# Kernel tuning notes

Hardware: AMD Instinct MI355X
Metric: run time of the kernel (lower is better)

The kernel has to match this reference:

```python
import jax, jax.numpy as jnp
import numpy as np

SIZE = 256
D_IN = 256
EPS = 1e-3  # keras BatchNormalization default epsilon


def _mlp(x, W1, b1, W2, b2):
    # smallMLP: Dense(size, relu) -> Dense(size)
    return jax.nn.relu(x @ W1 + b1) @ W2 + b2


def setup_inputs() -> dict:
    key = jax.random.key(0)
    ks = jax.random.split(key, 20)
    B, L1, L2 = 16, 1024, 1024
    s = 0.02
    inp = {
        "seq1M": jax.random.normal(ks[0], (B, L1, D_IN), jnp.float32),
        "seq2M": jax.random.normal(ks[1], (B, L2, D_IN), jnp.float32),
        "distogram": jax.random.uniform(ks[2], (B, L1, L2), jnp.float32),
        # shared K/Q/V smallMLP params (same layers applied to seq1 and seq2)
        "kW1": jax.random.normal(ks[3], (D_IN, SIZE), jnp.float32) * s,
        "kb1": jnp.zeros((SIZE,), jnp.float32),
        "kW2": jax.random.normal(ks[4], (SIZE, SIZE), jnp.float32) * s,
        "kb2": jnp.zeros((SIZE,), jnp.float32),
        "qW1": jax.random.normal(ks[5], (D_IN, SIZE), jnp.float32) * s,
        "qb1": jnp.zeros((SIZE,), jnp.float32),
        "qW2": jax.random.normal(ks[6], (SIZE, SIZE), jnp.float32) * s,
        "qb2": jnp.zeros((SIZE,), jnp.float32),
        "vW1": jax.random.normal(ks[7], (D_IN, SIZE), jnp.float32) * s,
        "vb1": jnp.zeros((SIZE,), jnp.float32),
        "vW2": jax.random.normal(ks[8], (SIZE, SIZE), jnp.float32) * s,
        "vb2": jnp.zeros((SIZE,), jnp.float32),
        # output projections
        "fc1W": jax.random.normal(ks[9], (SIZE, SIZE), jnp.float32) * s,
        "fc1b": jnp.zeros((SIZE,), jnp.float32),
        "fc2W": jax.random.normal(ks[10], (SIZE, SIZE), jnp.float32) * s,
        "fc2b": jnp.zeros((SIZE,), jnp.float32),
        # shared BatchNorm (inference mode, moving stats)
        "bn_gamma": jnp.ones((SIZE,), jnp.float32),
        "bn_beta": jnp.zeros((SIZE,), jnp.float32),
        "bn_mean": jnp.zeros((SIZE,), jnp.float32),
        "bn_var": jnp.ones((SIZE,), jnp.float32),
    }
    return inp


def reference(seq1M, seq2M, distogram,
              kW1, kb1, kW2, kb2,
              qW1, qb1, qW2, qb2,
              vW1, vb1, vW2, vb2,
              fc1W, fc1b, fc2W, fc2b,
              bn_gamma, bn_beta, bn_mean, bn_var):
    size = jnp.float32(SIZE)
    k1 = _mlp(seq1M, kW1, kb1, kW2, kb2)   # [B, L1, S]
    q1 = _mlp(seq1M, qW1, qb1, qW2, qb2)
    v1 = _mlp(seq1M, vW1, vb1, vW2, vb2)
    k2 = _mlp(seq2M, kW1, kb1, kW2, kb2)   # [B, L2, S]
    q2 = _mlp(seq2M, qW1, qb1, qW2, qb2)
    v2 = _mlp(seq2M, vW1, vb1, vW2, vb2)

    # distogram-scaled scores, softmax over axis 1 (query axis — non-standard)
    scores1 = jnp.einsum('bls,bms->blm', q1, k2) * distogram / size  # [B, L1, L2]
    w1 = jax.nn.softmax(scores1, axis=1)
    scores2 = jnp.einsum('bms,bls->bml', q2, k1) * jnp.transpose(distogram, (0, 2, 1)) / size  # [B, L2, L1]
    w2 = jax.nn.softmax(scores2, axis=1)

    # transpose(matmul(V^T, W), [0,2,1]) == einsum contracting the softmax axis
    ap1 = jnp.einsum('bls,blm->bms', v1, w1)  # [B, L2, S]
    ap2 = jnp.einsum('bms,bml->bls', v2, w2)  # [B, L1, S]

    def bn(x):
        return (x - bn_mean) * jax.lax.rsqrt(bn_var + EPS) * bn_gamma + bn_beta

    out1 = bn(jax.nn.relu(ap1 @ fc1W + fc1b))
    out2 = bn(jax.nn.relu(ap2 @ fc2W + fc2b))
    return out1, out2
```

## Files before the change

kernel.cpp:

```cpp
#include <hip/hip_runtime.h>
#include <hip/hip_bf16.h>


typedef __attribute__((ext_vector_type(8))) short bf16x8;
typedef __attribute__((ext_vector_type(4))) float f32x4;
typedef unsigned short u16;

__device__ __forceinline__ unsigned int f2bfbits(float f) {
  union { float f; unsigned int i; } v; v.f = f;
  return (v.i + 0x7fffu + ((v.i >> 16) & 1u)) >> 16;
}
__device__ __forceinline__ unsigned int pk2(float a, float b) {
  return f2bfbits(a) | (f2bfbits(b) << 16);
}

__global__ void pack_wt(const float* __restrict__ w0, const float* __restrict__ w1,
                        const float* __restrict__ w2, const float* __restrict__ w3,
                        const float* __restrict__ w4, const float* __restrict__ w5,
                        const float* __restrict__ w6, const float* __restrict__ w7,
                        u16* __restrict__ out) {
  const float* wsel[8] = {w0, w1, w2, w3, w4, w5, w6, w7};
  const float* W = wsel[blockIdx.y];
  u16* o = out + (size_t)blockIdx.y * 65536;
  int i0 = blockIdx.x * 1024 + threadIdx.x * 4;
  int n = i0 >> 8, k = i0 & 255;
  float a = W[(k + 0) * 256 + n];
  float b = W[(k + 1) * 256 + n];
  float c = W[(k + 2) * 256 + n];
  float d = W[(k + 3) * 256 + n];
  uint2 pv;
  pv.x = pk2(a, b);
  pv.y = pk2(c, d);
  *(uint2*)(o + i0) = pv;
}

__global__ __launch_bounds__(256, 2)
void mlp3_fused(const float* __restrict__ seqA, const float* __restrict__ seqB,
                const u16* __restrict__ Wt8,
                const float* __restrict__ kb1, const float* __restrict__ kb2,
                const float* __restrict__ qb1, const float* __restrict__ qb2,
                const float* __restrict__ vb1, const float* __restrict__ vb2,
                u16* __restrict__ kA, u16* __restrict__ qA, u16* __restrict__ vA,
                u16* __restrict__ kB, u16* __restrict__ qB, u16* __restrict__ vB)
{
  __shared__ u16 As[64][256];
  __shared__ u16 Hl[64][256];

  const int tid = threadIdx.x;
  const int lane = tid & 63;
  const int w = tid >> 6;
  const int l15 = lane & 15, lq = lane >> 4;
  const int seqsel = blockIdx.x >> 8;
  const size_t m0 = (size_t)(blockIdx.x & 255) * 64;
  const float* __restrict__ seq = seqsel ? seqB : seqA;

  {
    const int row = tid >> 2, cg = tid & 3;
    const float* src = seq + (m0 + row) * 256 + cg * 64;
#pragma unroll
    for (int cc = 0; cc < 8; ++cc) {
      float4 f0 = *(const float4*)(src + cc * 8);
      float4 f1 = *(const float4*)(src + cc * 8 + 4);
      uint4 pk;
      pk.x = pk2(f0.x, f0.y);
      pk.y = pk2(f0.z, f0.w);
      pk.z = pk2(f1.x, f1.y);
      pk.w = pk2(f1.z, f1.w);
      const int ch = (cg * 8 + cc) ^ (row & 7);
      *(uint4*)&As[row][ch * 8] = pk;
    }
  }
  __syncthreads();

#pragma unroll
  for (int mlp = 0; mlp < 3; ++mlp) {
    const u16* __restrict__ W1 = Wt8 + (size_t)(mlp * 2) * 65536;
    const u16* __restrict__ W2 = Wt8 + (size_t)(mlp * 2 + 1) * 65536;
    const float* __restrict__ b1 = (mlp == 0) ? kb1 : (mlp == 1) ? qb1 : vb1;
    const float* __restrict__ b2 = (mlp == 0) ? kb2 : (mlp == 1) ? qb2 : vb2;
    u16* __restrict__ dst =
        (mlp == 0) ? (seqsel ? kB : kA) : (mlp == 1) ? (seqsel ? qB : qA) : (seqsel ? vB : vA);

    float b1v[4][4];
#pragma unroll
    for (int ni = 0; ni < 4; ++ni)
#pragma unroll
      for (int r = 0; r < 4; ++r) b1v[ni][r] = b1[w * 64 + ni * 16 + 4 * lq + r];
    float b2v[4];
#pragma unroll
    for (int ni = 0; ni < 4; ++ni) b2v[ni] = b2[w * 64 + ni * 16 + l15];

    f32x4 a1[4][4];
#pragma unroll
    for (int ni = 0; ni < 4; ++ni)
#pragma unroll
      for (int mj = 0; mj < 4; ++mj) a1[ni][mj] = (f32x4)0.0f;
#pragma unroll
    for (int ks = 0; ks < 8; ++ks) {
      bf16x8 wf[4], af[4];
#pragma unroll
      for (int ni = 0; ni < 4; ++ni)
        wf[ni] = *(const bf16x8*)(W1 + (size_t)(w * 64 + ni * 16 + l15) * 256 + ks * 32 + lq * 8);
#pragma unroll
      for (int mj = 0; mj < 4; ++mj) {
        const int row = mj * 16 + l15;
        const int ch = (ks * 4 + lq) ^ (row & 7);
        af[mj] = *(const bf16x8*)&As[row][ch * 8];
      }
#pragma unroll
      for (int ni = 0; ni < 4; ++ni)
#pragma unroll
        for (int mj = 0; mj < 4; ++mj)
          a1[ni][mj] = __builtin_amdgcn_mfma_f32_16x16x32_bf16(wf[ni], af[mj], a1[ni][mj], 0, 0, 0);
    }

    __syncthreads();
#pragma unroll
    for (int ni = 0; ni < 4; ++ni) {
      const int chl = w * 8 + ni * 2 + (lq >> 1);
#pragma unroll
      for (int mj = 0; mj < 4; ++mj) {
        const int m = mj * 16 + l15;
        float h0 = fmaxf(a1[ni][mj][0] + b1v[ni][0], 0.f);
        float h1 = fmaxf(a1[ni][mj][1] + b1v[ni][1], 0.f);
        float h2 = fmaxf(a1[ni][mj][2] + b1v[ni][2], 0.f);
        float h3 = fmaxf(a1[ni][mj][3] + b1v[ni][3], 0.f);
        uint2 pv;
        pv.x = pk2(h0, h1);
        pv.y = pk2(h2, h3);
        const int ch = chl ^ (m & 7);
        *(uint2*)&Hl[m][ch * 8 + (lq & 1) * 4] = pv;
      }
    }
    __syncthreads();

    f32x4 a2[4][4];
#pragma unroll
    for (int mi = 0; mi < 4; ++mi)
#pragma unroll
      for (int ni = 0; ni < 4; ++ni) a2[mi][ni] = (f32x4)0.0f;
#pragma unroll
    for (int ks = 0; ks < 8; ++ks) {
      bf16x8 wf[4], hf[4];
#pragma unroll
      for (int ni = 0; ni < 4; ++ni)
        wf[ni] = *(const bf16x8*)(W2 + (size_t)(w * 64 + ni * 16 + l15) * 256 + ks * 32 + lq * 8);
#pragma unroll
      for (int mi = 0; mi < 4; ++mi) {
        const int row = mi * 16 + l15;
        const int ch = (ks * 4 + lq) ^ (row & 7);
        hf[mi] = *(const bf16x8*)&Hl[row][ch * 8];
      }
#pragma unroll
      for (int mi = 0; mi < 4; ++mi)
#pragma unroll
        for (int ni = 0; ni < 4; ++ni)
          a2[mi][ni] = __builtin_amdgcn_mfma_f32_16x16x32_bf16(hf[mi], wf[ni], a2[mi][ni], 0, 0, 0);
    }

#pragma unroll
    for (int ni = 0; ni < 4; ++ni) {
      const int col = w * 64 + ni * 16 + l15;
      const float bb = b2v[ni];
#pragma unroll
      for (int mi = 0; mi < 4; ++mi) {
        const size_t grow0 = m0 + mi * 16 + 4 * lq;
        float z[4];
#pragma unroll
        for (int r = 0; r < 4; ++r) z[r] = a2[mi][ni][r] + bb;
        if (mlp != 2) {
#pragma unroll
          for (int r = 0; r < 4; ++r)
            dst[(grow0 + r) * 256 + col] = (u16)f2bfbits(z[r]);
        } else {
          uint2 pv;
          pv.x = pk2(z[0], z[1]);
          pv.y = pk2(z[2], z[3]);
          const size_t bb2 = grow0 >> 10, lrow = grow0 & 1023;
          *(uint2*)(dst + ((size_t)bb2 * 256 + col) * 1024 + lrow) = pv;
        }
      }
    }
  }
}

enum { EPI_RELU_BF16 = 0, EPI_BF16 = 1, EPI_VT = 2, EPI_BN = 3 };

template <bool AF32, int EPI>
__global__ __launch_bounds__(256, 2)
void gemm_mfma(const void* __restrict__ Aptr, const u16* __restrict__ Wt,
               const float* __restrict__ bias, void* __restrict__ Cout,
               const float* __restrict__ bn_g, const float* __restrict__ bn_b,
               const float* __restrict__ bn_m, const float* __restrict__ bn_v)
{
  __shared__ u16 As[128][64];
  __shared__ u16 Ws[64][64];
  const int tid = threadIdx.x;
  const int lane = tid & 63;
  const int w = tid >> 6;
  const int wr = w >> 1, wc = w & 1;
  const int l15 = lane & 15, lq = lane >> 4;
  const size_t bm = (size_t)blockIdx.x * 128;
  const int bn = blockIdx.y * 64;

  const int sar = tid >> 1, sah = tid & 1;
  const int swr = tid >> 2, swc = tid & 3;

  f32x4 acc[4][2];
#pragma unroll
  for (int mi = 0; mi < 4; ++mi)
#pragma unroll
    for (int ni = 0; ni < 2; ++ni) acc[mi][ni] = (f32x4)0.0f;

  for (int k0 = 0; k0 < 256; k0 += 64) {
    __syncthreads();
    if (AF32) {
      const float* A = (const float*)Aptr + (bm + sar) * 256 + k0 + sah * 32;
#pragma unroll
      for (int c = 0; c < 4; ++c) {
        float4 f0 = *(const float4*)(A + c * 8);
        float4 f1 = *(const float4*)(A + c * 8 + 4);
        uint4 pk;
        pk.x = pk2(f0.x, f0.y);
        pk.y = pk2(f0.z, f0.w);
        pk.z = pk2(f1.x, f1.y);
        pk.w = pk2(f1.z, f1.w);
        int cc = (sah * 4 + c) ^ (sar & 7);
        *(uint4*)&As[sar][cc * 8] = pk;
      }
    } else {
      const u16* A = (const u16*)Aptr + (bm + sar) * 256 + k0 + sah * 32;
#pragma unroll
      for (int c = 0; c < 4; ++c) {
        uint4 v = *(const uint4*)(A + c * 8);
        int cc = (sah * 4 + c) ^ (sar & 7);
        *(uint4*)&As[sar][cc * 8] = v;
      }
    }
    {
      const u16* Wp = Wt + (size_t)(bn + swr) * 256 + k0 + swc * 16;
#pragma unroll
      for (int c = 0; c < 2; ++c) {
        uint4 v = *(const uint4*)(Wp + c * 8);
        int cc = (swc * 2 + c) ^ (swr & 7);
        *(uint4*)&Ws[swr][cc * 8] = v;
      }
    }
    __syncthreads();
#pragma unroll
    for (int ks = 0; ks < 2; ++ks) {
      bf16x8 af[4], wf[2];
#pragma unroll
      for (int mi = 0; mi < 4; ++mi) {
        int row = wr * 64 + mi * 16 + l15;
        int cc = (ks * 4 + lq) ^ (row & 7);
        af[mi] = *(const bf16x8*)&As[row][cc * 8];
      }
#pragma unroll
      for (int ni = 0; ni < 2; ++ni) {
        int row = wc * 32 + ni * 16 + l15;
        int cc = (ks * 4 + lq) ^ (row & 7);
        wf[ni] = *(const bf16x8*)&Ws[row][cc * 8];
      }
#pragma unroll
      for (int mi = 0; mi < 4; ++mi)
#pragma unroll
        for (int ni = 0; ni < 2; ++ni)
          acc[mi][ni] = __builtin_amdgcn_mfma_f32_16x16x32_bf16(
              af[mi], wf[ni], acc[mi][ni], 0, 0, 0);
    }
  }

#pragma unroll
  for (int ni = 0; ni < 2; ++ni) {
    const int col = bn + wc * 32 + ni * 16 + l15;
    const float bi = bias[col];
    float g = 0.f, be = 0.f, mu = 0.f, iv = 0.f;
    if (EPI == EPI_BN) {
      g = bn_g[col];
      be = bn_b[col];
      mu = bn_m[col];
      iv = rsqrtf(bn_v[col] + 1e-3f);
    }
#pragma unroll
    for (int mi = 0; mi < 4; ++mi) {
      const size_t grow0 = bm + wr * 64 + mi * 16 + 4 * lq;
      float z[4];
#pragma unroll
      for (int r = 0; r < 4; ++r) z[r] = acc[mi][ni][r] + bi;
      if (EPI == EPI_RELU_BF16) {
#pragma unroll
        for (int r = 0; r < 4; ++r)
          ((u16*)Cout)[(grow0 + r) * 256 + col] = (u16)f2bfbits(fmaxf(z[r], 0.f));
      } else if (EPI == EPI_BF16) {
#pragma unroll
        for (int r = 0; r < 4; ++r)
          ((u16*)Cout)[(grow0 + r) * 256 + col] = (u16)f2bfbits(z[r]);
      } else if (EPI == EPI_VT) {
        uint2 pv;
        pv.x = pk2(z[0], z[1]);
        pv.y = pk2(z[2], z[3]);
        const size_t b = grow0 >> 10, lrow = grow0 & 1023;
        *(uint2*)((u16*)Cout + ((size_t)b * 256 + col) * 1024 + lrow) = pv;
      } else {
#pragma unroll
        for (int r = 0; r < 4; ++r) {
          float zz = fmaxf(z[r], 0.f);
          ((float*)Cout)[(grow0 + r) * 256 + col] = (zz - mu) * iv * g + be;
        }
      }
    }
  }
}

__global__ __launch_bounds__(256, 2)
void attn_mfma(const u16* __restrict__ Qa, const u16* __restrict__ Ka,
               const u16* __restrict__ Va, u16* __restrict__ OutA,
               const u16* __restrict__ Qb, const u16* __restrict__ Kb,
               const u16* __restrict__ Vb, u16* __restrict__ OutB,
               const float* __restrict__ D2)
{
  __shared__ union U {
    struct {
      u16 Ks[2][32][256];
      u16 Vts[2][256][32];
      u16 Pl[64][40];
    } s;
    u16 Osw[4][16][264];
  } u;

  const int orig = blockIdx.x;
  const int lid = (orig & 7) * 64 + (orig >> 3);
  const int dir = lid >> 8;
  const int b = (lid >> 4) & 15;
  const int i0 = (lid & 15) * 64;

  const u16* __restrict__ Q = dir ? Qb : Qa;
  const u16* __restrict__ K = dir ? Kb : Ka;
  const u16* __restrict__ Vt = dir ? Vb : Va;
  u16* __restrict__ Out = dir ? OutB : OutA;

  const int tid = threadIdx.x;
  const int lane = tid & 63;
  const int w = tid >> 6;
  const int l15 = lane & 15, lq = lane >> 4;
  const size_t sbase = (size_t)b * (1024 * 256);
  const size_t vtbase = (size_t)b * (256 * 1024);
  const size_t dbase = (size_t)b * (1024 * 1024);

  bf16x8 q[8];
  {
    const u16* Qp = Q + sbase + (size_t)(i0 + w * 16 + l15) * 256 + lq * 8;
#pragma unroll
    for (int ks = 0; ks < 8; ++ks) q[ks] = *(const bf16x8*)(Qp + ks * 32);
  }

  const int cb0 = w * 4;
  auto stage = [&](int bi, int j0) {
#pragma unroll
    for (int i = 0; i < 4; ++i) {
      const int cb = cb0 + i;
      {
        const int krow = cb * 2 + (lane >> 5);
        const int kch = (lane & 31) ^ (krow & 7);
        const u16* gs = K + sbase + (size_t)(j0 + krow) * 256 + kch * 8;
        __builtin_amdgcn_global_load_lds(
            (const __attribute__((address_space(1))) unsigned int*)gs,
            (__attribute__((address_space(3))) unsigned int*)&u.s.Ks[bi][cb * 2][0],
            16, 0, 0);
      }
      {
        const int vrow = cb * 16 + (lane >> 2);
        const int vch = lane & 3;
        const u16* gs = Vt + vtbase + (size_t)vrow * 1024 + j0 + ((vch ^ (vrow & 3)) * 8);
        __builtin_amdgcn_global_load_lds(
            (const __attribute__((address_space(1))) unsigned int*)gs,
            (__attribute__((address_space(3))) unsigned int*)&u.s.Vts[bi][cb * 16][0],
            16, 0, 0);
      }
    }
  };

  float mrow[4], lsum[4];
  f32x4 o[16];
#pragma unroll
  for (int r = 0; r < 4; ++r) { mrow[r] = -1e30f; lsum[r] = 0.f; }
#pragma unroll
  for (int nt = 0; nt < 16; ++nt) o[nt] = (f32x4)0.0f;

  stage(0, 0);

  const int vcc = lq ^ (l15 & 3);

  for (int t = 0; t < 32; ++t) {
    const int bi = t & 1;
    const int j0 = t * 32;

    float breg[8];
    if (dir == 0) {
#pragma unroll
      for (int nt = 0; nt < 2; ++nt)
#pragma unroll
        for (int r = 0; r < 4; ++r)
          breg[nt * 4 + r] =
              D2[dbase + (size_t)(j0 + l15 + 16 * nt) * 1024 + (i0 + w * 16 + 4 * lq + r)];
    } else {
#pragma unroll
      for (int nt = 0; nt < 2; ++nt)
#pragma unroll
        for (int r = 0; r < 4; ++r)
          breg[nt * 4 + r] =
              D2[dbase + (size_t)(i0 + w * 16 + 4 * lq + r) * 1024 + j0 + l15 + 16 * nt];
    }

    if (t + 1 < 32) {
      stage(bi ^ 1, j0 + 32);
      asm volatile("s_waitcnt vmcnt(16)" ::: "memory");
    } else {
      asm volatile("s_waitcnt vmcnt(0)" ::: "memory");
    }
    __builtin_amdgcn_s_barrier();
    __builtin_amdgcn_sched_barrier(0);

    f32x4 sa[2];
    sa[0] = (f32x4)0.0f;
    sa[1] = (f32x4)0.0f;
#pragma unroll
    for (int ks = 0; ks < 8; ++ks)
#pragma unroll
      for (int nt = 0; nt < 2; ++nt) {
        const int row = nt * 16 + l15;
        const int cc = (ks * 4 + lq) ^ (row & 7);
        bf16x8 kb = *(const bf16x8*)&u.s.Ks[bi][row][cc * 8];
        sa[nt] = __builtin_amdgcn_mfma_f32_16x16x32_bf16(q[ks], kb, sa[nt], 0, 0, 0);
      }

    float s0[4], s1[4];
    bool need = false;
#pragma unroll
    for (int r = 0; r < 4; ++r) {
      s0[r] = sa[0][r] * breg[r] * 0.00390625f;
      s1[r] = sa[1][r] * breg[4 + r] * 0.00390625f;
      need = need || (s0[r] > mrow[r] + 8.f) || (s1[r] > mrow[r] + 8.f);
    }
    if (__any(need)) {
#pragma unroll
      for (int r = 0; r < 4; ++r) {
        float mx = fmaxf(s0[r], s1[r]);
        mx = fmaxf(mx, __shfl_xor(mx, 1, 16));
        mx = fmaxf(mx, __shfl_xor(mx, 2, 16));
        mx = fmaxf(mx, __shfl_xor(mx, 4, 16));
        mx = fmaxf(mx, __shfl_xor(mx, 8, 16));
        const float mn = fmaxf(mrow[r], mx);
        const float sc = __expf(mrow[r] - mn);
        mrow[r] = mn;
        lsum[r] *= sc;
#pragma unroll
        for (int nt = 0; nt < 16; ++nt) o[nt][r] *= sc;
      }
    }
    float p0v[4], p1v[4];
#pragma unroll
    for (int r = 0; r < 4; ++r) {
      p0v[r] = __expf(s0[r] - mrow[r]);
      p1v[r] = __expf(s1[r] - mrow[r]);
      lsum[r] += p0v[r] + p1v[r];
    }
#pragma unroll
    for (int r = 0; r < 4; ++r) {
      const int qrow = w * 16 + 4 * lq + r;
      u.s.Pl[qrow][l15] = (u16)f2bfbits(p0v[r]);
      u.s.Pl[qrow][16 + l15] = (u16)f2bfbits(p1v[r]);
    }
    __threadfence_block();
    const bf16x8 pa = *(const bf16x8*)&u.s.Pl[w * 16 + l15][lq * 8];

#pragma unroll
    for (int nt = 0; nt < 16; ++nt) {
      bf16x8 vb = *(const bf16x8*)&u.s.Vts[bi][nt * 16 + l15][vcc * 8];
      o[nt] = __builtin_amdgcn_mfma_f32_16x16x32_bf16(pa, vb, o[nt], 0, 0, 0);
    }

    asm volatile("s_waitcnt lgkmcnt(0)" ::: "memory");
    __builtin_amdgcn_s_barrier();
  }

  float inv[4];
#pragma unroll
  for (int r = 0; r < 4; ++r) {
    float rs = lsum[r];
    rs += __shfl_xor(rs, 1, 16);
    rs += __shfl_xor(rs, 2, 16);
    rs += __shfl_xor(rs, 4, 16);
    rs += __shfl_xor(rs, 8, 16);
    inv[r] = 1.0f / rs;
  }
#pragma unroll
  for (int nt = 0; nt < 16; ++nt) {
#pragma unroll
    for (int r = 0; r < 4; ++r)
      u.Osw[w][4 * lq + r][nt * 16 + l15] = (u16)f2bfbits(o[nt][r] * inv[r]);
  }
  __threadfence_block();
  {
    const int orow = lane >> 2, och = (lane & 3) * 64;
    const u16* src = &u.Osw[w][orow][och];
    u16* dst = Out + sbase + (size_t)(i0 + w * 16 + orow) * 256 + och;
#pragma unroll
    for (int c = 0; c < 8; ++c) *(uint4*)(dst + c * 8) = *(const uint4*)(src + c * 8);
  }
}

extern "C" void kernel_launch(void* const* d_in, const int* in_sizes, int n_in,
                              void* d_out, int out_size, void* d_ws, size_t ws_size,
                              hipStream_t stream)
{
  (void)in_sizes; (void)n_in; (void)out_size; (void)ws_size;

  const float* seq1  = (const float*)d_in[0];
  const float* seq2  = (const float*)d_in[1];
  const float* disto = (const float*)d_in[2];
  const float* kW1 = (const float*)d_in[3];
  const float* kb1 = (const float*)d_in[4];
  const float* kW2 = (const float*)d_in[5];
  const float* kb2 = (const float*)d_in[6];
  const float* qW1 = (const float*)d_in[7];
  const float* qb1 = (const float*)d_in[8];
  const float* qW2 = (const float*)d_in[9];
  const float* qb2 = (const float*)d_in[10];
  const float* vW1 = (const float*)d_in[11];
  const float* vb1 = (const float*)d_in[12];
  const float* vW2 = (const float*)d_in[13];
  const float* vb2 = (const float*)d_in[14];
  const float* fc1W = (const float*)d_in[15];
  const float* fc1b = (const float*)d_in[16];
  const float* fc2W = (const float*)d_in[17];
  const float* fc2b = (const float*)d_in[18];
  const float* bn_g = (const float*)d_in[19];
  const float* bn_b = (const float*)d_in[20];
  const float* bn_m = (const float*)d_in[21];
  const float* bn_v = (const float*)d_in[22];

  char* ws = (char*)d_ws;
  const size_t MB = 1024 * 1024;
  u16* Wt8 = (u16*)(ws);
  u16* k1  = (u16*)(ws + 1 * MB);
  u16* q1  = (u16*)(ws + 9 * MB);
  u16* k2  = (u16*)(ws + 17 * MB);
  u16* q2  = (u16*)(ws + 25 * MB);
  u16* v1t = (u16*)(ws + 33 * MB);
  u16* v2t = (u16*)(ws + 41 * MB);
  u16* ap1 = (u16*)(ws + 49 * MB);
  u16* ap2 = (u16*)(ws + 57 * MB);

  pack_wt<<<dim3(64, 8), 256, 0, stream>>>(kW1, kW2, qW1, qW2, vW1, vW2, fc1W, fc2W, Wt8);

  mlp3_fused<<<dim3(512), dim3(256), 0, stream>>>(
      seq1, seq2, Wt8, kb1, kb2, qb1, qb2, vb1, vb2,
      k1, q1, v1t, k2, q2, v2t);

  attn_mfma<<<dim3(512), dim3(256), 0, stream>>>(
      k2, q1, v1t, ap1,
      k1, q2, v2t, ap2,
      disto);

  float* out1 = (float*)d_out;
  float* out2 = (float*)d_out + 4194304;
  dim3 ggrid(128, 4), gblk(256);
  gemm_mfma<false, EPI_BN><<<ggrid, gblk, 0, stream>>>(
      ap1, Wt8 + 6ull * 65536, fc1b, (void*)out1, bn_g, bn_b, bn_m, bn_v);
  gemm_mfma<false, EPI_BN><<<ggrid, gblk, 0, stream>>>(
      ap2, Wt8 + 7ull * 65536, fc2b, (void*)out2, bn_g, bn_b, bn_m, bn_v);
}
```

Measured before the change: 184.0 us.

## Vectorize transposed distogram loads via LDS transpose, add MFMA priority hints

For direction 0, where the distogram tile is read transposed, each lane now issues two float4 loads along the contiguous dimension instead of eight scattered scalar loads, then transposes the values through a small per-wave LDS buffer. The vmcnt wait is adjusted to match the smaller number of outstanding loads. s_setprio raises wave priority around both MFMA loops, and __threadfence_block is replaced by an explicit lgkmcnt wait plus sched_barrier. The extra LDS use may lower occupancy, and the LDS round-trip adds latency.

```diff
diff --git a/kernel.cpp b/kernel.cpp
--- a/kernel.cpp
+++ b/kernel.cpp
@@ -325,6 +325,7 @@
       u16 Ks[2][32][256];
       u16 Vts[2][256][32];
       u16 Pl[64][40];
+      float Pw[4][32][20];
     } s;
     u16 Osw[4][16][264];
   } u;
@@ -391,19 +392,18 @@
   stage(0, 0);
 
   const int vcc = lq ^ (l15 & 3);
+  const int bj = lane & 31, bh = lane >> 5;
 
   for (int t = 0; t < 32; ++t) {
     const int bi = t & 1;
     const int j0 = t * 32;
 
     float breg[8];
+    float4 bb0, bb1;
     if (dir == 0) {
-#pragma unroll
-      for (int nt = 0; nt < 2; ++nt)
-#pragma unroll
-        for (int r = 0; r < 4; ++r)
-          breg[nt * 4 + r] =
-              D2[dbase + (size_t)(j0 + l15 + 16 * nt) * 1024 + (i0 + w * 16 + 4 * lq + r)];
+      const float* bsrc = D2 + dbase + (size_t)(j0 + bj) * 1024 + i0 + w * 16 + bh * 8;
+      bb0 = *(const float4*)bsrc;
+      bb1 = *(const float4*)(bsrc + 4);
     } else {
 #pragma unroll
       for (int nt = 0; nt < 2; ++nt)
@@ -415,16 +415,26 @@
 
     if (t + 1 < 32) {
       stage(bi ^ 1, j0 + 32);
-      asm volatile("s_waitcnt vmcnt(16)" ::: "memory");
+      if (dir == 0)
+        asm volatile("s_waitcnt vmcnt(10)" ::: "memory");
+      else
+        asm volatile("s_waitcnt vmcnt(16)" ::: "memory");
     } else {
       asm volatile("s_waitcnt vmcnt(0)" ::: "memory");
     }
     __builtin_amdgcn_s_barrier();
     __builtin_amdgcn_sched_barrier(0);
+
+    if (dir == 0) {
+      float* pw = &u.s.Pw[w][bj][bh * 8];
+      *(float4*)pw = bb0;
+      *(float4*)(pw + 4) = bb1;
+    }
 
     f32x4 sa[2];
     sa[0] = (f32x4)0.0f;
     sa[1] = (f32x4)0.0f;
+    __builtin_amdgcn_s_setprio(1);
 #pragma unroll
     for (int ks = 0; ks < 8; ++ks)
 #pragma unroll
@@ -434,13 +444,22 @@
         bf16x8 kb = *(const bf16x8*)&u.s.Ks[bi][row][cc * 8];
         sa[nt] = __builtin_amdgcn_mfma_f32_16x16x32_bf16(q[ks], kb, sa[nt], 0, 0, 0);
       }
+    __builtin_amdgcn_s_setprio(0);
 
     float s0[4], s1[4];
     bool need = false;
 #pragma unroll
     for (int r = 0; r < 4; ++r) {
-      s0[r] = sa[0][r] * breg[r] * 0.00390625f;
-      s1[r] = sa[1][r] * breg[4 + r] * 0.00390625f;
+      float b0, b1;
+      if (dir == 0) {
+        b0 = u.s.Pw[w][l15][4 * lq + r];
+        b1 = u.s.Pw[w][l15 + 16][4 * lq + r];
+      } else {
+        b0 = breg[r];
+        b1 = breg[4 + r];
+      }
+      s0[r] = sa[0][r] * b0 * 0.00390625f;
+      s1[r] = sa[1][r] * b1 * 0.00390625f;
       need = need || (s0[r] > mrow[r] + 8.f) || (s1[r] > mrow[r] + 8.f);
     }
     if (__any(need)) {
@@ -472,14 +491,17 @@
       u.s.Pl[qrow][l15] = (u16)f2bfbits(p0v[r]);
       u.s.Pl[qrow][16 + l15] = (u16)f2bfbits(p1v[r]);
     }
-    __threadfence_block();
+    asm volatile("s_waitcnt lgkmcnt(0)" ::: "memory");
+    __builtin_amdgcn_sched_barrier(0);
     const bf16x8 pa = *(const bf16x8*)&u.s.Pl[w * 16 + l15][lq * 8];
 
+    __builtin_amdgcn_s_setprio(1);
 #pragma unroll
     for (int nt = 0; nt < 16; ++nt) {
       bf16x8 vb = *(const bf16x8*)&u.s.Vts[bi][nt * 16 + l15][vcc * 8];
       o[nt] = __builtin_amdgcn_mfma_f32_16x16x32_bf16(pa, vb, o[nt], 0, 0, 0);
     }
+    __builtin_amdgcn_s_setprio(0);
 
     asm volatile("s_waitcnt lgkmcnt(0)" ::: "memory");
     __builtin_amdgcn_s_barrier();
@@ -501,7 +523,8 @@
     for (int r = 0; r < 4; ++r)
       u.Osw[w][4 * lq + r][nt * 16 + l15] = (u16)f2bfbits(o[nt][r] * inv[r]);
   }
-  __threadfence_block();
+  asm volatile("s_waitcnt lgkmcnt(0)" ::: "memory");
+  __builtin_amdgcn_sched_barrier(0);
   {
     const int orow = lane >> 2, och = (lane & 3) * 64;
     const u16* src = &u.Osw[w][orow][och];
```

Measured after the change: 261.1 us. 41.9% more time.

## Pre-transpose distogram to bf16 and restructure K/V staging in attention

Applied to the files above, without the earlier changes.

Adds a pack_disto kernel that transposes the distogram to bf16, so direction-0 attention reads it row-contiguously instead of with strided column reads. V staging becomes single-buffered and is issued at the start of each iteration, with a mid-iteration barrier and vmcnt waits replacing the fence, so V loads overlap the QK MFMAs. It also raises wave priority around the MFMA blocks with s_setprio. This trades an extra full pass over the 64MB distogram plus bf16 rounding of the scale against cheaper loads and less LDS inside the attention loop.

```diff
diff --git a/kernel.cpp b/kernel.cpp
--- a/kernel.cpp
+++ b/kernel.cpp
@@ -12,6 +12,11 @@
 }
 __device__ __forceinline__ unsigned int pk2(float a, float b) {
   return f2bfbits(a) | (f2bfbits(b) << 16);
+}
+__device__ __forceinline__ float bf2f(u16 x) {
+  union { unsigned int i; float f; } v;
+  v.i = (unsigned int)x << 16;
+  return v.f;
 }
 
 __global__ void pack_wt(const float* __restrict__ w0, const float* __restrict__ w1,
@@ -34,6 +39,32 @@
   *(uint2*)(o + i0) = pv;
 }
 
+__global__ __launch_bounds__(256)
+void pack_disto(const float* __restrict__ D, u16* __restrict__ Dt) {
+  __shared__ u16 T[64][72];
+  const int b = blockIdx.z, l0 = blockIdx.y * 64, m0 = blockIdx.x * 64;
+  const float* src = D + (size_t)b * (1024 * 1024);
+  u16* dst = Dt + (size_t)b * (1024 * 1024);
+  const int r = threadIdx.x >> 2, c0 = (threadIdx.x & 3) * 16;
+  float4 f[4];
+#pragma unroll
+  for (int q = 0; q < 4; ++q)
+    f[q] = *(const float4*)(src + (size_t)(l0 + r) * 1024 + m0 + c0 + q * 4);
+  uint4 p0, p1;
+  p0.x = pk2(f[0].x, f[0].y); p0.y = pk2(f[0].z, f[0].w);
+  p0.z = pk2(f[1].x, f[1].y); p0.w = pk2(f[1].z, f[1].w);
+  p1.x = pk2(f[2].x, f[2].y); p1.y = pk2(f[2].z, f[2].w);
+  p1.z = pk2(f[3].x, f[3].y); p1.w = pk2(f[3].z, f[3].w);
+  *(uint4*)&T[r][c0] = p0;
+  *(uint4*)&T[r][c0 + 8] = p1;
+  __syncthreads();
+  u16 vals[16];
+#pragma unroll
+  for (int k = 0; k < 16; ++k) vals[k] = T[c0 + k][r];
+  *(uint4*)(dst + (size_t)(m0 + r) * 1024 + l0 + c0) = *(uint4*)&vals[0];
+  *(uint4*)(dst + (size_t)(m0 + r) * 1024 + l0 + c0 + 8) = *(uint4*)&vals[8];
+}
+
 __global__ __launch_bounds__(256, 2)
 void mlp3_fused(const float* __restrict__ seqA, const float* __restrict__ seqB,
                 const u16* __restrict__ Wt8,
@@ -318,12 +349,12 @@
                const u16* __restrict__ Va, u16* __restrict__ OutA,
                const u16* __restrict__ Qb, const u16* __restrict__ Kb,
                const u16* __restrict__ Vb, u16* __restrict__ OutB,
-               const float* __restrict__ D2)
+               const u16* __restrict__ D1t, const float* __restrict__ D2)
 {
   __shared__ union U {
     struct {
       u16 Ks[2][32][256];
-      u16 Vts[2][256][32];
+      u16 Vts[256][32];
       u16 Pl[64][40];
     } s;
     u16 Osw[4][16][264];
@@ -356,28 +387,30 @@
   }
 
   const int cb0 = w * 4;
-  auto stage = [&](int bi, int j0) {
+  auto stage_K = [&](int bi, int j0) {
 #pragma unroll
     for (int i = 0; i < 4; ++i) {
       const int cb = cb0 + i;
-      {
-        const int krow = cb * 2 + (lane >> 5);
-        const int kch = (lane & 31) ^ (krow & 7);
-        const u16* gs = K + sbase + (size_t)(j0 + krow) * 256 + kch * 8;
-        __builtin_amdgcn_global_load_lds(
-            (const __attribute__((address_space(1))) unsigned int*)gs,
-            (__attribute__((address_space(3))) unsigned int*)&u.s.Ks[bi][cb * 2][0],
-            16, 0, 0);
-      }
-      {
-        const int vrow = cb * 16 + (lane >> 2);
-        const int vch = lane & 3;
-        const u16* gs = Vt + vtbase + (size_t)vrow * 1024 + j0 + ((vch ^ (vrow & 3)) * 8);
-        __builtin_amdgcn_global_load_lds(
-            (const __attribute__((address_space(1))) unsigned int*)gs,
-            (__attribute__((address_space(3))) unsigned int*)&u.s.Vts[bi][cb * 16][0],
-            16, 0, 0);
-      }
+      const int krow = cb * 2 + (lane >> 5);
+      const int kch = (lane & 31) ^ (krow & 7);
+      const u16* gs = K + sbase + (size_t)(j0 + krow) * 256 + kch * 8;
+      __builtin_amdgcn_global_load_lds(
+          (const __attribute__((address_space(1))) unsigned int*)gs,
+          (__attribute__((address_space(3))) unsigned int*)&u.s.Ks[bi][cb * 2][0],
+          16, 0, 0);
+    }
+  };
+  auto stage_V = [&](int j0) {
+#pragma unroll
+    for (int i = 0; i < 4; ++i) {
+      const int cb = cb0 + i;
+      const int vrow = cb * 16 + (lane >> 2);
+      const int vch = lane & 3;
+      const u16* gs = Vt + vtbase + (size_t)vrow * 1024 + j0 + ((vch ^ (vrow & 3)) * 8);
+      __builtin_amdgcn_global_load_lds(
+          (const __attribute__((address_space(1))) unsigned int*)gs,
+          (__attribute__((address_space(3))) unsigned int*)&u.s.Vts[cb * 16][0],
+          16, 0, 0);
     }
   };
 
@@ -388,7 +421,7 @@
 #pragma unroll
   for (int nt = 0; nt < 16; ++nt) o[nt] = (f32x4)0.0f;
 
-  stage(0, 0);
+  stage_K(0, 0);
 
   const int vcc = lq ^ (l15 & 3);
 
@@ -396,28 +429,31 @@
     const int bi = t & 1;
     const int j0 = t * 32;
 
-    float breg[8];
+    u16 bregu[8];
+    float bregf[8];
     if (dir == 0) {
 #pragma unroll
       for (int nt = 0; nt < 2; ++nt)
 #pragma unroll
         for (int r = 0; r < 4; ++r)
-          breg[nt * 4 + r] =
-              D2[dbase + (size_t)(j0 + l15 + 16 * nt) * 1024 + (i0 + w * 16 + 4 * lq + r)];
+          bregu[nt * 4 + r] =
+              D1t[dbase + (size_t)(i0 + w * 16 + 4 * lq + r) * 1024 + j0 + l15 + 16 * nt];
     } else {
 #pragma unroll
       for (int nt = 0; nt < 2; ++nt)
 #pragma unroll
         for (int r = 0; r < 4; ++r)
-          breg[nt * 4 + r] =
+          bregf[nt * 4 + r] =
               D2[dbase + (size_t)(i0 + w * 16 + 4 * lq + r) * 1024 + j0 + l15 + 16 * nt];
     }
 
+    stage_V(j0);
+    __builtin_amdgcn_sched_barrier(0);
     if (t + 1 < 32) {
-      stage(bi ^ 1, j0 + 32);
+      stage_K(bi ^ 1, j0 + 32);
       asm volatile("s_waitcnt vmcnt(16)" ::: "memory");
     } else {
-      asm volatile("s_waitcnt vmcnt(0)" ::: "memory");
+      asm volatile("s_waitcnt vmcnt(12)" ::: "memory");
     }
     __builtin_amdgcn_s_barrier();
     __builtin_amdgcn_sched_barrier(0);
@@ -425,6 +461,7 @@
     f32x4 sa[2];
     sa[0] = (f32x4)0.0f;
     sa[1] = (f32x4)0.0f;
+    __builtin_amdgcn_s_setprio(1);
 #pragma unroll
     for (int ks = 0; ks < 8; ++ks)
 #pragma unroll
@@ -434,13 +471,16 @@
         bf16x8 kb = *(const bf16x8*)&u.s.Ks[bi][row][cc * 8];
         sa[nt] = __builtin_amdgcn_mfma_f32_16x16x32_bf16(q[ks], kb, sa[nt], 0, 0, 0);
       }
+    __builtin_amdgcn_s_setprio(0);
 
     float s0[4], s1[4];
     bool need = false;
 #pragma unroll
     for (int r = 0; r < 4; ++r) {
-      s0[r] = sa[0][r] * breg[r] * 0.00390625f;
-      s1[r] = sa[1][r] * breg[4 + r] * 0.00390625f;
+      const float b0 = (dir == 0) ? bf2f(bregu[r]) : bregf[r];
+      const float b1 = (dir == 0) ? bf2f(bregu[4 + r]) : bregf[4 + r];
+      s0[r] = sa[0][r] * b0 * 0.00390625f;
+      s1[r] = sa[1][r] * b1 * 0.00390625f;
       need = need || (s0[r] > mrow[r] + 8.f) || (s1[r] > mrow[r] + 8.f);
     }
     if (__any(need)) {
@@ -472,14 +512,21 @@
       u.s.Pl[qrow][l15] = (u16)f2bfbits(p0v[r]);
       u.s.Pl[qrow][16 + l15] = (u16)f2bfbits(p1v[r]);
     }
-    __threadfence_block();
+    if (t + 1 < 32)
+      asm volatile("s_waitcnt vmcnt(4) lgkmcnt(0)" ::: "memory");
+    else
+      asm volatile("s_waitcnt vmcnt(0) lgkmcnt(0)" ::: "memory");
+    __builtin_amdgcn_sched_barrier(0);
+    __builtin_amdgcn_s_barrier();
     const bf16x8 pa = *(const bf16x8*)&u.s.Pl[w * 16 + l15][lq * 8];
 
+    __builtin_amdgcn_s_setprio(1);
 #pragma unroll
     for (int nt = 0; nt < 16; ++nt) {
-      bf16x8 vb = *(const bf16x8*)&u.s.Vts[bi][nt * 16 + l15][vcc * 8];
+      bf16x8 vb = *(const bf16x8*)&u.s.Vts[nt * 16 + l15][vcc * 8];
       o[nt] = __builtin_amdgcn_mfma_f32_16x16x32_bf16(pa, vb, o[nt], 0, 0, 0);
     }
+    __builtin_amdgcn_s_setprio(0);
 
     asm volatile("s_waitcnt lgkmcnt(0)" ::: "memory");
     __builtin_amdgcn_s_barrier();
@@ -501,7 +548,8 @@
     for (int r = 0; r < 4; ++r)
       u.Osw[w][4 * lq + r][nt * 16 + l15] = (u16)f2bfbits(o[nt][r] * inv[r]);
   }
-  __threadfence_block();
+  asm volatile("s_waitcnt lgkmcnt(0)" ::: "memory");
+  __builtin_amdgcn_sched_barrier(0);
   {
     const int orow = lane >> 2, och = (lane & 3) * 64;
     const u16* src = &u.Osw[w][orow][och];
@@ -552,8 +600,10 @@
   u16* v2t = (u16*)(ws + 41 * MB);
   u16* ap1 = (u16*)(ws + 49 * MB);
   u16* ap2 = (u16*)(ws + 57 * MB);
+  u16* D1t = (u16*)(ws + 65 * MB);
 
   pack_wt<<<dim3(64, 8), 256, 0, stream>>>(kW1, kW2, qW1, qW2, vW1, vW2, fc1W, fc2W, Wt8);
+  pack_disto<<<dim3(16, 16, 16), 256, 0, stream>>>(disto, D1t);
 
   mlp3_fused<<<dim3(512), dim3(256), 0, stream>>>(
       seq1, seq2, Wt8, kb1, kb2, qb1, qb2, vb1, vb2,
@@ -562,7 +612,7 @@
   attn_mfma<<<dim3(512), dim3(256), 0, stream>>>(
       k2, q1, v1t, ap1,
       k1, q2, v2t, ap2,
-      disto);
+      D1t, disto);
 
   float* out1 = (float*)d_out;
   float* out2 = (float*)d_out + 4194304;
```

After: 174.1 us. 1.06x faster.
